# Kernel tuning notes

Hardware: AMD Instinct MI355X
Metric: run time of the kernel (lower is better)

The kernel has to match this reference:

```python
import jax, jax.numpy as jnp
import numpy as np

D_MODEL = 512
NUM_HEADS = 8
DEPTH = D_MODEL // NUM_HEADS


def setup_inputs() -> dict:
    key = jax.random.key(0)
    kx, kq, kk, kv, ko = jax.random.split(key, 5)
    scale = 1.0 / np.sqrt(D_MODEL)
    return {
        "x": jax.random.normal(kx, (4, 2048, D_MODEL), dtype=jnp.float32),
        "W_q": jax.random.normal(kq, (D_MODEL, D_MODEL), dtype=jnp.float32) * scale,
        "W_k": jax.random.normal(kk, (D_MODEL, D_MODEL), dtype=jnp.float32) * scale,
        "W_v": jax.random.normal(kv, (D_MODEL, D_MODEL), dtype=jnp.float32) * scale,
        "W_o": jax.random.normal(ko, (D_MODEL, D_MODEL), dtype=jnp.float32) * scale,
    }


def reference(x, W_q, W_k, W_v, W_o):
    B, S, _ = x.shape
    # nn.Linear with weight W: y = x @ W.T
    def split_heads(t):
        return t.reshape(B, S, NUM_HEADS, DEPTH).transpose(0, 2, 1, 3)  # [B,H,S,D]
    Q = split_heads(x @ W_q.T)
    K = split_heads(x @ W_k.T)
    V = split_heads(x @ W_v.T)
    b = -jnp.log(jnp.asarray(S, dtype=jnp.float32))  # -log(seq_len) bias
    inv_sqrt_dk = 1.0 / jnp.sqrt(jnp.asarray(DEPTH, dtype=jnp.float32))
    qk = jnp.einsum('bhqd,bhkd->bhqk', Q, K) * inv_sqrt_dk
    attn = jax.nn.sigmoid(qk + b)  # non-softmax sigmoid attention
    out = jnp.einsum('bhqk,bhkd->bhqd', attn, V)
    out = out.transpose(0, 2, 1, 3).reshape(B, S, D_MODEL)
    return out @ W_o.T
```

## Files before the change

kernel.cpp:

```cpp
#include <hip/hip_runtime.h>
#include <stdint.h>

typedef _Float16 f16x8 __attribute__((ext_vector_type(8)));
typedef _Float16 f16x4 __attribute__((ext_vector_type(4)));
typedef __fp16 h16x2 __attribute__((ext_vector_type(2)));
typedef float f32x4 __attribute__((ext_vector_type(4)));

#define SEQ 2048
#define NHEADS 8

#define GLOAD_LDS16(gp, lp)                                                        \
  __builtin_amdgcn_global_load_lds(                                                \
      (const __attribute__((address_space(1))) void*)(uintptr_t)(const void*)(gp), \
      (__attribute__((address_space(3))) void*)(uintptr_t)(void*)(lp), 16, 0, 0)

__device__ __forceinline__ void barrier_lds() {
  __builtin_amdgcn_s_waitcnt(0xc07f);
  __builtin_amdgcn_s_barrier();
}

__device__ __forceinline__ f16x4 pack4(float a, float b, float c, float d) {
  h16x2 lo = __builtin_amdgcn_cvt_pkrtz(a, b);
  h16x2 hi = __builtin_amdgcn_cvt_pkrtz(c, d);
  f16x4 o;
  o.x = (_Float16)lo.x; o.y = (_Float16)lo.y;
  o.z = (_Float16)hi.x; o.w = (_Float16)hi.y;
  return o;
}

__global__ void cvt_all_kernel(const float* __restrict__ x, const float* __restrict__ wq,
                               const float* __restrict__ wk, const float* __restrict__ wv,
                               const float* __restrict__ wo, _Float16* __restrict__ xh,
                               _Float16* __restrict__ wh) {
  int i = blockIdx.x * 256 + threadIdx.x;
  const float* src;
  _Float16* dst;
  int off;
  if (i < 1048576) {
    src = x; dst = xh; off = i;
  } else {
    int j = i - 1048576;
    int sel = j >> 16;
    off = j & 65535;
    src = (sel == 0) ? wq : (sel == 1) ? wk : (sel == 2) ? wv : wo;
    dst = wh + (size_t)sel * 262144;
  }
  float4 v = ((const float4*)src)[off];
  ((f16x4*)dst)[off] = pack4(v.x, v.y, v.z, v.w);
}

__device__ __forceinline__ void gemm_tile_bt(const _Float16* __restrict__ A,
                                             const _Float16* __restrict__ B,
                                             int m0, int n0,
                                             _Float16* As, _Float16* Bs,
                                             f32x4 (&acc)[4][4]) {
  const int tid = threadIdx.x;
  const int w = tid >> 6, lane = tid & 63;
  const int wr = w >> 1, wc = w & 1;
  const int lrow = lane & 15, q = lane >> 4;
  const int snb = w * 32 + (lane >> 3);
  const int scb = lane & 7;

#pragma unroll
  for (int i = 0; i < 4; ++i)
#pragma unroll
    for (int j = 0; j < 4; ++j)
#pragma unroll
      for (int r = 0; r < 4; ++r) acc[i][j][r] = 0.f;

  for (int kt = 0; kt < 8; ++kt) {
    __syncthreads();
#pragma unroll
    for (int t = 0; t < 4; ++t) {
      int n = snb + t * 8;
      int cbg = scb ^ (n & 7);
      GLOAD_LDS16(A + (size_t)(m0 + n) * 512 + kt * 64 + cbg * 8,
                  As + (w * 32 + t * 8) * 64);
      GLOAD_LDS16(B + (size_t)(n0 + n) * 512 + kt * 64 + cbg * 8,
                  Bs + (w * 32 + t * 8) * 64);
    }
    __syncthreads();

    f16x8 af[4][2], bfr[4][2];
#pragma unroll
    for (int i = 0; i < 4; ++i) {
      int m = wr * 64 + i * 16 + lrow;
#pragma unroll
      for (int kk = 0; kk < 2; ++kk) {
        int cb = (kk * 4 + q) ^ (m & 7);
        af[i][kk] = *(const f16x8*)(As + m * 64 + cb * 8);
      }
    }
#pragma unroll
    for (int j = 0; j < 4; ++j) {
      int n = wc * 64 + j * 16 + lrow;
#pragma unroll
      for (int kk = 0; kk < 2; ++kk) {
        int cb = (kk * 4 + q) ^ (n & 7);
        bfr[j][kk] = *(const f16x8*)(Bs + n * 64 + cb * 8);
      }
    }
#pragma unroll
    for (int i = 0; i < 4; ++i)
#pragma unroll
      for (int j = 0; j < 4; ++j) {
        acc[i][j] = __builtin_amdgcn_mfma_f32_16x16x32_f16(af[i][0], bfr[j][0], acc[i][j], 0, 0, 0);
        acc[i][j] = __builtin_amdgcn_mfma_f32_16x16x32_f16(af[i][1], bfr[j][1], acc[i][j], 0, 0, 0);
      }
  }
}

__global__ __launch_bounds__(256, 2) void qkv_kernel(
    const _Float16* __restrict__ xb, const _Float16* __restrict__ Wq,
    const _Float16* __restrict__ Wk, const _Float16* __restrict__ Wv,
    _Float16* __restrict__ Qo, _Float16* __restrict__ Ko, _Float16* __restrict__ Vto) {
  __shared__ _Float16 pool[17408];
  _Float16* As = pool;
  _Float16* Bs = pool + 8192;
  const int z = blockIdx.z;
  f32x4 acc[4][4];
  const int tid = threadIdx.x, w = tid >> 6, lane = tid & 63;
  const int wr = w >> 1, wc = w & 1, lcol = lane & 15, q = lane >> 4;

  if (z < 2) {
    const int m0 = blockIdx.y * 128;
    const int n0 = blockIdx.x * 128;
    gemm_tile_bt((z == 0) ? Wq : Wk, xb, m0, n0, As, Bs, acc);
    _Float16* outp = (z == 0) ? Qo : Ko;
    __syncthreads();
#pragma unroll
    for (int i = 0; i < 4; ++i) {
      int cl = wr * 64 + i * 16 + q * 4;
#pragma unroll
      for (int j = 0; j < 4; ++j) {
        int s = wc * 64 + j * 16 + lcol;
        *(f16x4*)(pool + s * 136 + cl) =
            pack4(acc[i][j][0], acc[i][j][1], acc[i][j][2], acc[i][j][3]);
      }
    }
    __syncthreads();
#pragma unroll
    for (int it = 0; it < 16; ++it) {
      int srow = it * 8 + (tid >> 5);
      int ch = tid & 31;
      f16x4 v = *(const f16x4*)(pool + srow * 136 + ch * 4);
      *(f16x4*)(outp + (size_t)(n0 + srow) * 512 + m0 + ch * 4) = v;
    }
  } else {
    const int m0 = blockIdx.x * 128;
    const int n0 = blockIdx.y * 128;
    gemm_tile_bt(xb, Wv, m0, n0, As, Bs, acc);
    const int bb = m0 >> 11, sl0 = m0 & 2047;
    __syncthreads();
#pragma unroll
    for (int i = 0; i < 4; ++i) {
      int s0 = wr * 64 + i * 16 + q * 4;
#pragma unroll
      for (int j = 0; j < 4; ++j) {
        int c = wc * 64 + j * 16 + lcol;
        *(f16x4*)(pool + c * 136 + s0) =
            pack4(acc[i][j][0], acc[i][j][1], acc[i][j][2], acc[i][j][3]);
      }
    }
    __syncthreads();
#pragma unroll
    for (int it = 0; it < 16; ++it) {
      int crow = it * 8 + (tid >> 5);
      int ch = tid & 31;
      int cg = n0 + crow, h = cg >> 6, d = cg & 63;
      f16x4 v = *(const f16x4*)(pool + crow * 136 + ch * 4);
      *(f16x4*)(Vto + ((size_t)((bb * NHEADS + h) * 64 + d)) * SEQ + sl0 + ch * 4) = v;
    }
  }
}

__global__ __launch_bounds__(256, 2) void attn_kernel(
    const _Float16* __restrict__ Qw, const _Float16* __restrict__ Kw,
    const _Float16* __restrict__ Vtw, _Float16* __restrict__ Ow) {
  __shared__ _Float16 lds[32768];
  _Float16* Ps = lds;
  _Float16* Qs = lds;
  _Float16* Ks = lds + 16384;
  _Float16* Vts = lds + 24576;

  const int tid = threadIdx.x, w = tid >> 6, lane = tid & 63;
  const int lrow = lane & 15, q = lane >> 4;

  const int L = blockIdx.x;
  const int xcd = L & 7, slot = L >> 3;
  const int bh = xcd * 4 + (slot >> 4), qt = slot & 15;
  const int b = bh >> 3, h = bh & 7;
  const int q0 = qt * 128;

  const _Float16* Qp = Qw + ((size_t)(b * SEQ + q0)) * 512 + h * 64;
  const _Float16* Kp = Kw + ((size_t)b * SEQ) * 512 + h * 64;
  const _Float16* Vp = Vtw + (size_t)bh * 64 * SEQ;

  const int snb = w * 32 + (lane >> 3), scb = lane & 7;
  const int vnb = w * 16 + (lane >> 4), vcb = lane & 15;

#pragma unroll
  for (int t = 0; t < 4; ++t) {
    int n = snb + t * 8;
    int cbg = scb ^ (n & 7);
    GLOAD_LDS16(Qp + (size_t)n * 512 + cbg * 8, Qs + (w * 32 + t * 8) * 64);
  }
  __syncthreads();

  f16x8 qa[2][2];
#pragma unroll
  for (int i = 0; i < 2; ++i) {
    int m = w * 32 + i * 16 + lrow;
#pragma unroll
    for (int kk = 0; kk < 2; ++kk) {
      int cb = (kk * 4 + q) ^ (m & 7);
      qa[i][kk] = *(const f16x8*)(Qs + m * 64 + cb * 8);
    }
  }
  barrier_lds();

  f32x4 oacc[2][4];
#pragma unroll
  for (int i = 0; i < 2; ++i)
#pragma unroll
    for (int j = 0; j < 4; ++j)
#pragma unroll
      for (int r = 0; r < 4; ++r) oacc[i][j][r] = 0.f;

  const float c1 = 0.18033688011112042f;

  for (int kt = 0; kt < 16; ++kt) {
    barrier_lds();
#pragma unroll
    for (int t = 0; t < 4; ++t) {
      int n = snb + t * 8;
      int cbg = scb ^ (n & 7);
      GLOAD_LDS16(Kp + (size_t)(kt * 128 + n) * 512 + cbg * 8, Ks + (w * 32 + t * 8) * 64);
    }
#pragma unroll
    for (int t = 0; t < 4; ++t) {
      int nv = vnb + t * 4;
      int cbg = vcb ^ (nv & 15);
      GLOAD_LDS16(Vp + (size_t)nv * SEQ + kt * 128 + cbg * 8, Vts + (w * 16 + t * 4) * 128);
    }
    __syncthreads();

#pragma unroll
    for (int j = 0; j < 8; ++j) {
      int n = j * 16 + lrow;
      int cb0 = q ^ (n & 7), cb1 = (4 + q) ^ (n & 7);
      f16x8 k0 = *(const f16x8*)(Ks + n * 64 + cb0 * 8);
      f16x8 k1 = *(const f16x8*)(Ks + n * 64 + cb1 * 8);
      f32x4 s0, s1;
#pragma unroll
      for (int r = 0; r < 4; ++r) { s0[r] = 0.f; s1[r] = 0.f; }
      s0 = __builtin_amdgcn_mfma_f32_16x16x32_f16(k0, qa[0][0], s0, 0, 0, 0);
      s0 = __builtin_amdgcn_mfma_f32_16x16x32_f16(k1, qa[0][1], s0, 0, 0, 0);
      s1 = __builtin_amdgcn_mfma_f32_16x16x32_f16(k0, qa[1][0], s1, 0, 0, 0);
      s1 = __builtin_amdgcn_mfma_f32_16x16x32_f16(k1, qa[1][1], s1, 0, 0, 0);

      int kbase = j * 16 + q * 4;
      int kb8 = j * 2 + (q >> 1);
#pragma unroll
      for (int i = 0; i < 2; ++i) {
        int qrow = w * 32 + i * 16 + lrow;
        float p[4];
#pragma unroll
        for (int r = 0; r < 4; ++r) {
          float sv = (i == 0) ? s0[r] : s1[r];
          float wp = __builtin_amdgcn_exp2f(__builtin_fmaf(sv, c1, -1.0f));
          float e = wp * 0.0009765625f;
          float t1 = __builtin_fmaf(e, e, -e);
          p[r] = __builtin_fmaf(wp, t1, wp);
        }
        *(f16x4*)(Ps + qrow * 128 + ((kb8 ^ (qrow & 15)) << 3) + (kbase & 7)) =
            pack4(p[0], p[1], p[2], p[3]);
      }
    }

#pragma unroll
    for (int ks = 0; ks < 4; ++ks) {
      int m0r = w * 32 + lrow, m1r = m0r + 16;
      f16x8 pa0 = *(const f16x8*)(Ps + m0r * 128 + (((ks * 4 + q) ^ (m0r & 15)) << 3));
      f16x8 pa1 = *(const f16x8*)(Ps + m1r * 128 + (((ks * 4 + q) ^ (m1r & 15)) << 3));
      f16x8 vb[4];
#pragma unroll
      for (int j2 = 0; j2 < 4; ++j2) {
        int n = j2 * 16 + lrow;
        vb[j2] = *(const f16x8*)(Vts + n * 128 + (((ks * 4 + q) ^ (n & 15)) << 3));
      }
#pragma unroll
      for (int j2 = 0; j2 < 4; ++j2) {
        oacc[0][j2] = __builtin_amdgcn_mfma_f32_16x16x32_f16(pa0, vb[j2], oacc[0][j2], 0, 0, 0);
        oacc[1][j2] = __builtin_amdgcn_mfma_f32_16x16x32_f16(pa1, vb[j2], oacc[1][j2], 0, 0, 0);
      }
    }
  }

  barrier_lds();
  _Float16* Ob = Ps;
#pragma unroll
  for (int i2 = 0; i2 < 2; ++i2) {
#pragma unroll
    for (int j2 = 0; j2 < 4; ++j2) {
      int d = j2 * 16 + lrow;
#pragma unroll
      for (int r = 0; r < 4; ++r) {
        int row = w * 32 + i2 * 16 + q * 4 + r;
        Ob[row * 72 + d] = (_Float16)(oacc[i2][j2][r] * 0.0009765625f);
      }
    }
  }
  barrier_lds();
#pragma unroll
  for (int it = 0; it < 8; ++it) {
    int row = it * 16 + (tid >> 4);
    int ch = tid & 15;
    f16x4 v = *(const f16x4*)(Ob + row * 72 + ch * 4);
    *(f16x4*)(Ow + (size_t)(b * SEQ + q0 + row) * 512 + h * 64 + ch * 4) = v;
  }
}

__global__ __launch_bounds__(256, 2) void oproj_kernel(
    const _Float16* __restrict__ A, const _Float16* __restrict__ Wo,
    float* __restrict__ out) {
  __shared__ _Float16 As[128 * 64];
  __shared__ _Float16 Bs[128 * 64];
  const int m0 = blockIdx.x * 128, n0 = blockIdx.y * 128;
  f32x4 acc[4][4];
  gemm_tile_bt(A, Wo, m0, n0, As, Bs, acc);

  const int tid = threadIdx.x, w = tid >> 6, lane = tid & 63;
  const int wr = w >> 1, wc = w & 1, lcol = lane & 15, q = lane >> 4;
#pragma unroll
  for (int i = 0; i < 4; ++i) {
    int gm0 = m0 + wr * 64 + i * 16 + q * 4;
#pragma unroll
    for (int j = 0; j < 4; ++j) {
      int gn = n0 + wc * 64 + j * 16 + lcol;
#pragma unroll
      for (int r = 0; r < 4; ++r)
        out[(size_t)(gm0 + r) * 512 + gn] = acc[i][j][r];
    }
  }
}

extern "C" void kernel_launch(void* const* d_in, const int* in_sizes, int n_in,
                              void* d_out, int out_size, void* d_ws, size_t ws_size,
                              hipStream_t stream) {
  const float* x = (const float*)d_in[0];
  const float* Wq = (const float*)d_in[1];
  const float* Wk = (const float*)d_in[2];
  const float* Wv = (const float*)d_in[3];
  const float* Wo = (const float*)d_in[4];
  float* out = (float*)d_out;
  char* ws = (char*)d_ws;

  _Float16* xh = (_Float16*)(ws + 0);
  _Float16* wh = (_Float16*)(ws + 8388608);
  _Float16* Qw = (_Float16*)(ws + 10485760);
  _Float16* Kw = (_Float16*)(ws + 18874368);
  _Float16* Vtw = (_Float16*)(ws + 27262976);
  _Float16* Ow = (_Float16*)(ws + 35651584);

  _Float16* wqh = wh;
  _Float16* wkh = wh + 262144;
  _Float16* wvh = wh + 524288;
  _Float16* woh = wh + 786432;

  cvt_all_kernel<<<5120, 256, 0, stream>>>(x, Wq, Wk, Wv, Wo, xh, wh);
  qkv_kernel<<<dim3(64, 4, 3), 256, 0, stream>>>(xh, wqh, wkh, wvh, Qw, Kw, Vtw);
  attn_kernel<<<512, 256, 0, stream>>>(Qw, Kw, Vtw, Ow);
  oproj_kernel<<<dim3(64, 4), 256, 0, stream>>>(Ow, woh, out);
}
```

Measured before the change: 153.0 us.

## Double-buffer LDS tiles and keep sigmoid probabilities in registers for PV MFMA

The shared GEMM tile routine and the attention kernel now use two LDS buffers. The next K-slab (or K/V tile) is prefetched with global_load_lds while the current one is consumed, which drops one barrier per iteration and overlaps global loads with MFMA work. In attention, the sigmoid outputs are no longer written to LDS and re-read. They are packed straight from the QK^T accumulator layout into the A operand of 16x16x16 MFMAs against V, which removes an LDS round trip and its bank traffic. In exchange, LDS use per block rises to 64KB and the PV product is issued as more, smaller MFMAs.

```diff
diff --git a/kernel.cpp b/kernel.cpp
--- a/kernel.cpp
+++ b/kernel.cpp
@@ -52,7 +52,7 @@
 __device__ __forceinline__ void gemm_tile_bt(const _Float16* __restrict__ A,
                                              const _Float16* __restrict__ B,
                                              int m0, int n0,
-                                             _Float16* As, _Float16* Bs,
+                                             _Float16* lds,
                                              f32x4 (&acc)[4][4]) {
   const int tid = threadIdx.x;
   const int w = tid >> 6, lane = tid & 63;
@@ -68,18 +68,28 @@
 #pragma unroll
       for (int r = 0; r < 4; ++r) acc[i][j][r] = 0.f;
 
+#pragma unroll
+  for (int t = 0; t < 4; ++t) {
+    int n = snb + t * 8;
+    int cbg = scb ^ (n & 7);
+    GLOAD_LDS16(A + (size_t)(m0 + n) * 512 + cbg * 8, lds + (w * 32 + t * 8) * 64);
+    GLOAD_LDS16(B + (size_t)(n0 + n) * 512 + cbg * 8, lds + 8192 + (w * 32 + t * 8) * 64);
+  }
+
   for (int kt = 0; kt < 8; ++kt) {
     __syncthreads();
-#pragma unroll
-    for (int t = 0; t < 4; ++t) {
-      int n = snb + t * 8;
-      int cbg = scb ^ (n & 7);
-      GLOAD_LDS16(A + (size_t)(m0 + n) * 512 + kt * 64 + cbg * 8,
-                  As + (w * 32 + t * 8) * 64);
-      GLOAD_LDS16(B + (size_t)(n0 + n) * 512 + kt * 64 + cbg * 8,
-                  Bs + (w * 32 + t * 8) * 64);
-    }
-    __syncthreads();
+    if (kt < 7) {
+      _Float16* nb = lds + ((kt + 1) & 1) * 16384;
+#pragma unroll
+      for (int t = 0; t < 4; ++t) {
+        int n = snb + t * 8;
+        int cbg = scb ^ (n & 7);
+        GLOAD_LDS16(A + (size_t)(m0 + n) * 512 + (kt + 1) * 64 + cbg * 8, nb + (w * 32 + t * 8) * 64);
+        GLOAD_LDS16(B + (size_t)(n0 + n) * 512 + (kt + 1) * 64 + cbg * 8, nb + 8192 + (w * 32 + t * 8) * 64);
+      }
+    }
+    _Float16* As = lds + (kt & 1) * 16384;
+    _Float16* Bs = As + 8192;
 
     f16x8 af[4][2], bfr[4][2];
 #pragma unroll
@@ -114,9 +124,7 @@
     const _Float16* __restrict__ xb, const _Float16* __restrict__ Wq,
     const _Float16* __restrict__ Wk, const _Float16* __restrict__ Wv,
     _Float16* __restrict__ Qo, _Float16* __restrict__ Ko, _Float16* __restrict__ Vto) {
-  __shared__ _Float16 pool[17408];
-  _Float16* As = pool;
-  _Float16* Bs = pool + 8192;
+  __shared__ _Float16 pool[32768];
   const int z = blockIdx.z;
   f32x4 acc[4][4];
   const int tid = threadIdx.x, w = tid >> 6, lane = tid & 63;
@@ -125,7 +133,7 @@
   if (z < 2) {
     const int m0 = blockIdx.y * 128;
     const int n0 = blockIdx.x * 128;
-    gemm_tile_bt((z == 0) ? Wq : Wk, xb, m0, n0, As, Bs, acc);
+    gemm_tile_bt((z == 0) ? Wq : Wk, xb, m0, n0, pool, acc);
     _Float16* outp = (z == 0) ? Qo : Ko;
     __syncthreads();
 #pragma unroll
@@ -149,7 +157,7 @@
   } else {
     const int m0 = blockIdx.x * 128;
     const int n0 = blockIdx.y * 128;
-    gemm_tile_bt(xb, Wv, m0, n0, As, Bs, acc);
+    gemm_tile_bt(xb, Wv, m0, n0, pool, acc);
     const int bb = m0 >> 11, sl0 = m0 & 2047;
     __syncthreads();
 #pragma unroll
@@ -178,10 +186,6 @@
     const _Float16* __restrict__ Qw, const _Float16* __restrict__ Kw,
     const _Float16* __restrict__ Vtw, _Float16* __restrict__ Ow) {
   __shared__ _Float16 lds[32768];
-  _Float16* Ps = lds;
-  _Float16* Qs = lds;
-  _Float16* Ks = lds + 16384;
-  _Float16* Vts = lds + 24576;
 
   const int tid = threadIdx.x, w = tid >> 6, lane = tid & 63;
   const int lrow = lane & 15, q = lane >> 4;
@@ -199,6 +203,7 @@
   const int snb = w * 32 + (lane >> 3), scb = lane & 7;
   const int vnb = w * 16 + (lane >> 4), vcb = lane & 15;
 
+  _Float16* Qs = lds;
 #pragma unroll
   for (int t = 0; t < 4; ++t) {
     int n = snb + t * 8;
@@ -219,6 +224,19 @@
   }
   barrier_lds();
 
+#pragma unroll
+  for (int t = 0; t < 4; ++t) {
+    int n = snb + t * 8;
+    int cbg = scb ^ (n & 7);
+    GLOAD_LDS16(Kp + (size_t)n * 512 + cbg * 8, lds + (w * 32 + t * 8) * 64);
+  }
+#pragma unroll
+  for (int t = 0; t < 4; ++t) {
+    int nv = vnb + t * 4;
+    int cbg = vcb ^ (nv & 15);
+    GLOAD_LDS16(Vp + (size_t)nv * SEQ + cbg * 8, lds + 8192 + (w * 16 + t * 4) * 128);
+  }
+
   f32x4 oacc[2][4];
 #pragma unroll
   for (int i = 0; i < 2; ++i)
@@ -230,27 +248,30 @@
   const float c1 = 0.18033688011112042f;
 
   for (int kt = 0; kt < 16; ++kt) {
-    barrier_lds();
-#pragma unroll
-    for (int t = 0; t < 4; ++t) {
-      int n = snb + t * 8;
-      int cbg = scb ^ (n & 7);
-      GLOAD_LDS16(Kp + (size_t)(kt * 128 + n) * 512 + cbg * 8, Ks + (w * 32 + t * 8) * 64);
-    }
-#pragma unroll
-    for (int t = 0; t < 4; ++t) {
-      int nv = vnb + t * 4;
-      int cbg = vcb ^ (nv & 15);
-      GLOAD_LDS16(Vp + (size_t)nv * SEQ + kt * 128 + cbg * 8, Vts + (w * 16 + t * 4) * 128);
-    }
-    __syncthreads();
+    __syncthreads();
+    if (kt < 15) {
+      _Float16* nb = lds + ((kt + 1) & 1) * 16384;
+#pragma unroll
+      for (int t = 0; t < 4; ++t) {
+        int n = snb + t * 8;
+        int cbg = scb ^ (n & 7);
+        GLOAD_LDS16(Kp + (size_t)((kt + 1) * 128 + n) * 512 + cbg * 8, nb + (w * 32 + t * 8) * 64);
+      }
+#pragma unroll
+      for (int t = 0; t < 4; ++t) {
+        int nv = vnb + t * 4;
+        int cbg = vcb ^ (nv & 15);
+        GLOAD_LDS16(Vp + (size_t)nv * SEQ + (kt + 1) * 128 + cbg * 8, nb + 8192 + (w * 16 + t * 4) * 128);
+      }
+    }
+    _Float16* Ksc = lds + (kt & 1) * 16384;
+    _Float16* Vtsc = Ksc + 8192;
 
 #pragma unroll
     for (int j = 0; j < 8; ++j) {
       int n = j * 16 + lrow;
-      int cb0 = q ^ (n & 7), cb1 = (4 + q) ^ (n & 7);
-      f16x8 k0 = *(const f16x8*)(Ks + n * 64 + cb0 * 8);
-      f16x8 k1 = *(const f16x8*)(Ks + n * 64 + cb1 * 8);
+      f16x8 k0 = *(const f16x8*)(Ksc + n * 64 + ((q ^ (n & 7)) << 3));
+      f16x8 k1 = *(const f16x8*)(Ksc + n * 64 + (((4 + q) ^ (n & 7)) << 3));
       f32x4 s0, s1;
 #pragma unroll
       for (int r = 0; r < 4; ++r) { s0[r] = 0.f; s1[r] = 0.f; }
@@ -259,46 +280,32 @@
       s1 = __builtin_amdgcn_mfma_f32_16x16x32_f16(k0, qa[1][0], s1, 0, 0, 0);
       s1 = __builtin_amdgcn_mfma_f32_16x16x32_f16(k1, qa[1][1], s1, 0, 0, 0);
 
-      int kbase = j * 16 + q * 4;
-      int kb8 = j * 2 + (q >> 1);
-#pragma unroll
-      for (int i = 0; i < 2; ++i) {
-        int qrow = w * 32 + i * 16 + lrow;
-        float p[4];
-#pragma unroll
-        for (int r = 0; r < 4; ++r) {
-          float sv = (i == 0) ? s0[r] : s1[r];
-          float wp = __builtin_amdgcn_exp2f(__builtin_fmaf(sv, c1, -1.0f));
-          float e = wp * 0.0009765625f;
-          float t1 = __builtin_fmaf(e, e, -e);
-          p[r] = __builtin_fmaf(wp, t1, wp);
-        }
-        *(f16x4*)(Ps + qrow * 128 + ((kb8 ^ (qrow & 15)) << 3) + (kbase & 7)) =
-            pack4(p[0], p[1], p[2], p[3]);
-      }
-    }
-
-#pragma unroll
-    for (int ks = 0; ks < 4; ++ks) {
-      int m0r = w * 32 + lrow, m1r = m0r + 16;
-      f16x8 pa0 = *(const f16x8*)(Ps + m0r * 128 + (((ks * 4 + q) ^ (m0r & 15)) << 3));
-      f16x8 pa1 = *(const f16x8*)(Ps + m1r * 128 + (((ks * 4 + q) ^ (m1r & 15)) << 3));
-      f16x8 vb[4];
+      float p0[4], p1[4];
+#pragma unroll
+      for (int r = 0; r < 4; ++r) {
+        float wp = __builtin_amdgcn_exp2f(__builtin_fmaf(s0[r], c1, -1.0f));
+        float e = wp * 0.0009765625f;
+        p0[r] = __builtin_fmaf(wp, __builtin_fmaf(e, e, -e), wp);
+        float wp1 = __builtin_amdgcn_exp2f(__builtin_fmaf(s1[r], c1, -1.0f));
+        float e1 = wp1 * 0.0009765625f;
+        p1[r] = __builtin_fmaf(wp1, __builtin_fmaf(e1, e1, -e1), wp1);
+      }
+      f16x4 pf0 = pack4(p0[0], p0[1], p0[2], p0[3]);
+      f16x4 pf1 = pack4(p1[0], p1[1], p1[2], p1[3]);
+
 #pragma unroll
       for (int j2 = 0; j2 < 4; ++j2) {
-        int n = j2 * 16 + lrow;
-        vb[j2] = *(const f16x8*)(Vts + n * 128 + (((ks * 4 + q) ^ (n & 15)) << 3));
-      }
-#pragma unroll
-      for (int j2 = 0; j2 < 4; ++j2) {
-        oacc[0][j2] = __builtin_amdgcn_mfma_f32_16x16x32_f16(pa0, vb[j2], oacc[0][j2], 0, 0, 0);
-        oacc[1][j2] = __builtin_amdgcn_mfma_f32_16x16x32_f16(pa1, vb[j2], oacc[1][j2], 0, 0, 0);
+        int nv = j2 * 16 + lrow;
+        int cb = (j * 2 + (q >> 1)) ^ (nv & 15);
+        f16x4 vb = *(const f16x4*)(Vtsc + nv * 128 + (cb << 3) + ((q & 1) << 2));
+        oacc[0][j2] = __builtin_amdgcn_mfma_f32_16x16x16f16(pf0, vb, oacc[0][j2], 0, 0, 0);
+        oacc[1][j2] = __builtin_amdgcn_mfma_f32_16x16x16f16(pf1, vb, oacc[1][j2], 0, 0, 0);
       }
     }
   }
 
   barrier_lds();
-  _Float16* Ob = Ps;
+  _Float16* Ob = lds;
 #pragma unroll
   for (int i2 = 0; i2 < 2; ++i2) {
 #pragma unroll
@@ -324,11 +331,10 @@
 __global__ __launch_bounds__(256, 2) void oproj_kernel(
     const _Float16* __restrict__ A, const _Float16* __restrict__ Wo,
     float* __restrict__ out) {
-  __shared__ _Float16 As[128 * 64];
-  __shared__ _Float16 Bs[128 * 64];
+  __shared__ _Float16 pool[32768];
   const int m0 = blockIdx.x * 128, n0 = blockIdx.y * 128;
   f32x4 acc[4][4];
-  gemm_tile_bt(A, Wo, m0, n0, As, Bs, acc);
+  gemm_tile_bt(A, Wo, m0, n0, pool, acc);
 
   const int tid = threadIdx.x, w = tid >> 6, lane = tid & 63;
   const int wr = w >> 1, wc = w & 1, lcol = lane & 15, q = lane >> 4;
```

Result: no change. 152.5 us (-0.4%).

## Restructure attention to 64-row tiles with double-buffered K/V and register P

Applied to the files above, without the earlier changes.

The attention kernel now works on 64-query tiles with 64-key steps, doubling the grid, and double-buffers K/V loads so the next tile's global-to-LDS copy overlaps current compute. P stays in registers and feeds a 16x16x16 MFMA directly, which removes the LDS round trip for P. The sigmoid polynomial now runs in packed fp16, and the exp scale constant is folded into Q inside the QKV epilogue. Occupancy hints are raised as well. Risks are lower fp16 precision in the sigmoid approximation and a Q value rounded to fp16 after pre-scaling.

```diff
diff --git a/kernel.cpp b/kernel.cpp
--- a/kernel.cpp
+++ b/kernel.cpp
@@ -3,6 +3,7 @@
 
 typedef _Float16 f16x8 __attribute__((ext_vector_type(8)));
 typedef _Float16 f16x4 __attribute__((ext_vector_type(4)));
+typedef _Float16 f16v2 __attribute__((ext_vector_type(2)));
 typedef __fp16 h16x2 __attribute__((ext_vector_type(2)));
 typedef float f32x4 __attribute__((ext_vector_type(4)));
 
@@ -110,7 +111,7 @@
   }
 }
 
-__global__ __launch_bounds__(256, 2) void qkv_kernel(
+__global__ __launch_bounds__(256, 3) void qkv_kernel(
     const _Float16* __restrict__ xb, const _Float16* __restrict__ Wq,
     const _Float16* __restrict__ Wk, const _Float16* __restrict__ Wv,
     _Float16* __restrict__ Qo, _Float16* __restrict__ Ko, _Float16* __restrict__ Vto) {
@@ -126,6 +127,7 @@
     const int m0 = blockIdx.y * 128;
     const int n0 = blockIdx.x * 128;
     gemm_tile_bt((z == 0) ? Wq : Wk, xb, m0, n0, As, Bs, acc);
+    const float sc = (z == 0) ? 0.18033688011112042f : 1.0f;
     _Float16* outp = (z == 0) ? Qo : Ko;
     __syncthreads();
 #pragma unroll
@@ -135,7 +137,7 @@
       for (int j = 0; j < 4; ++j) {
         int s = wc * 64 + j * 16 + lcol;
         *(f16x4*)(pool + s * 136 + cl) =
-            pack4(acc[i][j][0], acc[i][j][1], acc[i][j][2], acc[i][j][3]);
+            pack4(acc[i][j][0] * sc, acc[i][j][1] * sc, acc[i][j][2] * sc, acc[i][j][3] * sc);
       }
     }
     __syncthreads();
@@ -174,146 +176,121 @@
   }
 }
 
-__global__ __launch_bounds__(256, 2) void attn_kernel(
+__global__ __launch_bounds__(256, 4) void attn_kernel(
     const _Float16* __restrict__ Qw, const _Float16* __restrict__ Kw,
     const _Float16* __restrict__ Vtw, _Float16* __restrict__ Ow) {
-  __shared__ _Float16 lds[32768];
-  _Float16* Ps = lds;
-  _Float16* Qs = lds;
-  _Float16* Ks = lds + 16384;
-  _Float16* Vts = lds + 24576;
+  __shared__ _Float16 lds[16384];
 
   const int tid = threadIdx.x, w = tid >> 6, lane = tid & 63;
   const int lrow = lane & 15, q = lane >> 4;
 
   const int L = blockIdx.x;
   const int xcd = L & 7, slot = L >> 3;
-  const int bh = xcd * 4 + (slot >> 4), qt = slot & 15;
+  const int bh = xcd * 4 + (slot >> 5), qt = slot & 31;
   const int b = bh >> 3, h = bh & 7;
-  const int q0 = qt * 128;
+  const int q0 = qt * 64;
 
   const _Float16* Qp = Qw + ((size_t)(b * SEQ + q0)) * 512 + h * 64;
   const _Float16* Kp = Kw + ((size_t)b * SEQ) * 512 + h * 64;
   const _Float16* Vp = Vtw + (size_t)bh * 64 * SEQ;
 
-  const int snb = w * 32 + (lane >> 3), scb = lane & 7;
-  const int vnb = w * 16 + (lane >> 4), vcb = lane & 15;
-
-#pragma unroll
-  for (int t = 0; t < 4; ++t) {
-    int n = snb + t * 8;
-    int cbg = scb ^ (n & 7);
-    GLOAD_LDS16(Qp + (size_t)n * 512 + cbg * 8, Qs + (w * 32 + t * 8) * 64);
+  const int sr = w * 16 + (lane >> 3);
+  const int scb = lane & 7;
+
+#pragma unroll
+  for (int t = 0; t < 2; ++t) {
+    int row = sr + t * 8;
+    int cbg = scb ^ (row & 7);
+    GLOAD_LDS16(Qp + (size_t)row * 512 + cbg * 8, lds + (w * 16 + t * 8) * 64);
   }
   __syncthreads();
 
-  f16x8 qa[2][2];
-#pragma unroll
-  for (int i = 0; i < 2; ++i) {
-    int m = w * 32 + i * 16 + lrow;
-#pragma unroll
-    for (int kk = 0; kk < 2; ++kk) {
-      int cb = (kk * 4 + q) ^ (m & 7);
-      qa[i][kk] = *(const f16x8*)(Qs + m * 64 + cb * 8);
-    }
+  f16x8 qa[2];
+  {
+    int m = w * 16 + lrow;
+#pragma unroll
+    for (int kk = 0; kk < 2; ++kk)
+      qa[kk] = *(const f16x8*)(lds + m * 64 + (((kk * 4 + q) ^ (m & 7)) << 3));
   }
   barrier_lds();
 
-  f32x4 oacc[2][4];
-#pragma unroll
-  for (int i = 0; i < 2; ++i)
-#pragma unroll
-    for (int j = 0; j < 4; ++j)
-#pragma unroll
-      for (int r = 0; r < 4; ++r) oacc[i][j][r] = 0.f;
-
-  const float c1 = 0.18033688011112042f;
-
-  for (int kt = 0; kt < 16; ++kt) {
-    barrier_lds();
-#pragma unroll
-    for (int t = 0; t < 4; ++t) {
-      int n = snb + t * 8;
-      int cbg = scb ^ (n & 7);
-      GLOAD_LDS16(Kp + (size_t)(kt * 128 + n) * 512 + cbg * 8, Ks + (w * 32 + t * 8) * 64);
-    }
-#pragma unroll
-    for (int t = 0; t < 4; ++t) {
-      int nv = vnb + t * 4;
-      int cbg = vcb ^ (nv & 15);
-      GLOAD_LDS16(Vp + (size_t)nv * SEQ + kt * 128 + cbg * 8, Vts + (w * 16 + t * 4) * 128);
-    }
-    __syncthreads();
-
-#pragma unroll
-    for (int j = 0; j < 8; ++j) {
+#pragma unroll
+  for (int t = 0; t < 2; ++t) {
+    int row = sr + t * 8;
+    int cbg = scb ^ (row & 7);
+    GLOAD_LDS16(Kp + (size_t)row * 512 + cbg * 8, lds + (w * 16 + t * 8) * 64);
+    GLOAD_LDS16(Vp + (size_t)row * SEQ + cbg * 8, lds + 4096 + (w * 16 + t * 8) * 64);
+  }
+
+  f32x4 oacc[4];
+#pragma unroll
+  for (int j = 0; j < 4; ++j)
+#pragma unroll
+    for (int r = 0; r < 4; ++r) oacc[j][r] = 0.f;
+
+  const f16v2 c2 = {(_Float16)4.8828125e-4f, (_Float16)4.8828125e-4f};
+
+  for (int kt = 0; kt < 32; ++kt) {
+    __syncthreads();
+    if (kt < 31) {
+      _Float16* nb = lds + ((kt + 1) & 1) * 8192;
+#pragma unroll
+      for (int t = 0; t < 2; ++t) {
+        int row = sr + t * 8;
+        int cbg = scb ^ (row & 7);
+        GLOAD_LDS16(Kp + (size_t)((kt + 1) * 64 + row) * 512 + cbg * 8, nb + (w * 16 + t * 8) * 64);
+        GLOAD_LDS16(Vp + (size_t)row * SEQ + (kt + 1) * 64 + cbg * 8, nb + 4096 + (w * 16 + t * 8) * 64);
+      }
+    }
+    const _Float16* Ksc = lds + (kt & 1) * 8192;
+    const _Float16* Vtsc = Ksc + 4096;
+
+#pragma unroll
+    for (int j = 0; j < 4; ++j) {
       int n = j * 16 + lrow;
-      int cb0 = q ^ (n & 7), cb1 = (4 + q) ^ (n & 7);
-      f16x8 k0 = *(const f16x8*)(Ks + n * 64 + cb0 * 8);
-      f16x8 k1 = *(const f16x8*)(Ks + n * 64 + cb1 * 8);
-      f32x4 s0, s1;
-#pragma unroll
-      for (int r = 0; r < 4; ++r) { s0[r] = 0.f; s1[r] = 0.f; }
-      s0 = __builtin_amdgcn_mfma_f32_16x16x32_f16(k0, qa[0][0], s0, 0, 0, 0);
-      s0 = __builtin_amdgcn_mfma_f32_16x16x32_f16(k1, qa[0][1], s0, 0, 0, 0);
-      s1 = __builtin_amdgcn_mfma_f32_16x16x32_f16(k0, qa[1][0], s1, 0, 0, 0);
-      s1 = __builtin_amdgcn_mfma_f32_16x16x32_f16(k1, qa[1][1], s1, 0, 0, 0);
-
-      int kbase = j * 16 + q * 4;
-      int kb8 = j * 2 + (q >> 1);
-#pragma unroll
-      for (int i = 0; i < 2; ++i) {
-        int qrow = w * 32 + i * 16 + lrow;
-        float p[4];
-#pragma unroll
-        for (int r = 0; r < 4; ++r) {
-          float sv = (i == 0) ? s0[r] : s1[r];
-          float wp = __builtin_amdgcn_exp2f(__builtin_fmaf(sv, c1, -1.0f));
-          float e = wp * 0.0009765625f;
-          float t1 = __builtin_fmaf(e, e, -e);
-          p[r] = __builtin_fmaf(wp, t1, wp);
-        }
-        *(f16x4*)(Ps + qrow * 128 + ((kb8 ^ (qrow & 15)) << 3) + (kbase & 7)) =
-            pack4(p[0], p[1], p[2], p[3]);
-      }
-    }
-
-#pragma unroll
-    for (int ks = 0; ks < 4; ++ks) {
-      int m0r = w * 32 + lrow, m1r = m0r + 16;
-      f16x8 pa0 = *(const f16x8*)(Ps + m0r * 128 + (((ks * 4 + q) ^ (m0r & 15)) << 3));
-      f16x8 pa1 = *(const f16x8*)(Ps + m1r * 128 + (((ks * 4 + q) ^ (m1r & 15)) << 3));
-      f16x8 vb[4];
+      f16x8 k0 = *(const f16x8*)(Ksc + n * 64 + ((q ^ (n & 7)) << 3));
+      f16x8 k1 = *(const f16x8*)(Ksc + n * 64 + (((4 + q) ^ (n & 7)) << 3));
+      f32x4 s;
+#pragma unroll
+      for (int r = 0; r < 4; ++r) s[r] = 0.f;
+      s = __builtin_amdgcn_mfma_f32_16x16x32_f16(k0, qa[0], s, 0, 0, 0);
+      s = __builtin_amdgcn_mfma_f32_16x16x32_f16(k1, qa[1], s, 0, 0, 0);
+
+      float u0 = __builtin_amdgcn_exp2f(s[0]);
+      float u1 = __builtin_amdgcn_exp2f(s[1]);
+      float u2 = __builtin_amdgcn_exp2f(s[2]);
+      float u3 = __builtin_amdgcn_exp2f(s[3]);
+      f16v2 ua = __builtin_bit_cast(f16v2, __builtin_amdgcn_cvt_pkrtz(u0, u1));
+      f16v2 ub = __builtin_bit_cast(f16v2, __builtin_amdgcn_cvt_pkrtz(u2, u3));
+      f16v2 wa = ua * c2, wb = ub * c2;
+      f16v2 ta = wa * wa - wa, tb = wb * wb - wb;
+      f16v2 pa2 = ua * ta + ua, pb2 = ub * tb + ub;
+      f16x4 pf;
+      pf.x = pa2.x; pf.y = pa2.y; pf.z = pb2.x; pf.w = pb2.y;
+
 #pragma unroll
       for (int j2 = 0; j2 < 4; ++j2) {
-        int n = j2 * 16 + lrow;
-        vb[j2] = *(const f16x8*)(Vts + n * 128 + (((ks * 4 + q) ^ (n & 15)) << 3));
-      }
-#pragma unroll
-      for (int j2 = 0; j2 < 4; ++j2) {
-        oacc[0][j2] = __builtin_amdgcn_mfma_f32_16x16x32_f16(pa0, vb[j2], oacc[0][j2], 0, 0, 0);
-        oacc[1][j2] = __builtin_amdgcn_mfma_f32_16x16x32_f16(pa1, vb[j2], oacc[1][j2], 0, 0, 0);
-      }
-    }
-  }
-
+        int nv = j2 * 16 + lrow;
+        int kbs = (j * 2 + (q >> 1)) ^ (nv & 7);
+        f16x4 vb = *(const f16x4*)(Vtsc + nv * 64 + (kbs << 3) + ((q & 1) << 2));
+        oacc[j2] = __builtin_amdgcn_mfma_f32_16x16x16f16(pf, vb, oacc[j2], 0, 0, 0);
+      }
+    }
+  }
+
+  _Float16* Ob = lds;
+#pragma unroll
+  for (int j2 = 0; j2 < 4; ++j2) {
+    int d = j2 * 16 + lrow;
+#pragma unroll
+    for (int r = 0; r < 4; ++r) {
+      int row = w * 16 + q * 4 + r;
+      Ob[row * 72 + d] = (_Float16)(oacc[j2][r] * 4.8828125e-4f);
+    }
+  }
   barrier_lds();
-  _Float16* Ob = Ps;
-#pragma unroll
-  for (int i2 = 0; i2 < 2; ++i2) {
-#pragma unroll
-    for (int j2 = 0; j2 < 4; ++j2) {
-      int d = j2 * 16 + lrow;
-#pragma unroll
-      for (int r = 0; r < 4; ++r) {
-        int row = w * 32 + i2 * 16 + q * 4 + r;
-        Ob[row * 72 + d] = (_Float16)(oacc[i2][j2][r] * 0.0009765625f);
-      }
-    }
-  }
-  barrier_lds();
-#pragma unroll
-  for (int it = 0; it < 8; ++it) {
+#pragma unroll
+  for (int it = 0; it < 4; ++it) {
     int row = it * 16 + (tid >> 4);
     int ch = tid & 15;
     f16x4 v = *(const f16x4*)(Ob + row * 72 + ch * 4);
@@ -324,11 +301,10 @@
 __global__ __launch_bounds__(256, 2) void oproj_kernel(
     const _Float16* __restrict__ A, const _Float16* __restrict__ Wo,
     float* __restrict__ out) {
-  __shared__ _Float16 As[128 * 64];
-  __shared__ _Float16 Bs[128 * 64];
+  __shared__ _Float16 pool[16384];
   const int m0 = blockIdx.x * 128, n0 = blockIdx.y * 128;
   f32x4 acc[4][4];
-  gemm_tile_bt(A, Wo, m0, n0, As, Bs, acc);
+  gemm_tile_bt(A, Wo, m0, n0, pool, pool + 8192, acc);
 
   const int tid = threadIdx.x, w = tid >> 6, lane = tid & 63;
   const int wr = w >> 1, wc = w & 1, lcol = lane & 15, q = lane >> 4;
@@ -370,6 +346,6 @@
 
   cvt_all_kernel<<<5120, 256, 0, stream>>>(x, Wq, Wk, Wv, Wo, xh, wh);
   qkv_kernel<<<dim3(64, 4, 3), 256, 0, stream>>>(xh, wqh, wkh, wvh, Qw, Kw, Vtw);
-  attn_kernel<<<512, 256, 0, stream>>>(Qw, Kw, Vtw, Ow);
+  attn_kernel<<<1024, 256, 0, stream>>>(Qw, Kw, Vtw, Ow);
   oproj_kernel<<<dim3(64, 4), 256, 0, stream>>>(Ow, woh, out);
 }
```

Measured after the change: 157.7 us. 3.0% more time.
